# Kernel tuning notes

Measured on AMD Instinct MI355X. Metric: run time of the kernel, lower is better.

The kernel has to match this reference:

```python
import jax, jax.numpy as jnp
import numpy as np

B, N, DIM, H = 512, 98, 512, 16
HD = DIM // H
WS = (2, 7, 7)  # window size; N == 2*7*7


def _relative_position_index(ws):
    d, h, w = ws
    coords = np.stack(np.meshgrid(np.arange(d), np.arange(h), np.arange(w), indexing='ij'))
    cf = coords.reshape(3, -1)  # [3, N]
    rel = cf[:, :, None] - cf[:, None, :]  # [3, N, N]
    rel = rel.transpose(1, 2, 0).astype(np.int64)
    rel[:, :, 0] += d - 1
    rel[:, :, 1] += h - 1
    rel[:, :, 2] += w - 1
    rel[:, :, 0] *= (2 * h - 1) * (2 * w - 1)
    rel[:, :, 1] *= 2 * w - 1
    return rel.sum(-1)  # [N, N] in [0, (2d-1)(2h-1)(2w-1))


def setup_inputs() -> dict:
    key = jax.random.key(0)
    ks = jax.random.split(key, 6)
    table_size = (2 * WS[0] - 1) * (2 * WS[1] - 1) * (2 * WS[2] - 1)  # 507
    return {
        'x': jax.random.normal(ks[0], (B, N, DIM), jnp.float32),
        'qkv_w': jax.random.normal(ks[1], (DIM, 3 * DIM), jnp.float32) * 0.02,
        'qkv_b': jnp.zeros((3 * DIM,), jnp.float32),
        'proj_w': jax.random.normal(ks[2], (DIM, DIM), jnp.float32) * 0.02,
        'proj_b': jnp.zeros((DIM,), jnp.float32),
        'bias_table': jax.random.normal(ks[3], (table_size, H), jnp.float32) * 0.02,
        'rel_index': jnp.asarray(_relative_position_index(WS)),
    }


def reference(x, qkv_w, qkv_b, proj_w, proj_b, bias_table, rel_index):
    b, n, c = x.shape
    scale = HD ** -0.5
    qkv = (x @ qkv_w + qkv_b).reshape(b, n, 3, H, HD)
    qkv = jnp.transpose(qkv, (2, 0, 3, 1, 4))  # [3, B, H, N, HD]
    q, k, v = qkv[0] * scale, qkv[1], qkv[2]
    attn = jnp.einsum('bhnd,bhmd->bhnm', q, k)  # [B, H, N, N]
    # gather relative position bias: [N,N] indices into [table, H] -> [H, N, N]
    bias = jnp.transpose(bias_table[rel_index], (2, 0, 1))
    attn = jax.nn.softmax(attn + bias[None], axis=-1)
    out = jnp.einsum('bhnm,bhmd->bhnd', attn, v)  # [B, H, N, HD]
    out = jnp.transpose(out, (0, 2, 1, 3)).reshape(b, n, c)
    return out @ proj_w + proj_b
```

## Files before the change

### kernel.cpp

```cpp
#include <hip/hip_runtime.h>

typedef unsigned short u16;
typedef __bf16 bf16x8 __attribute__((ext_vector_type(8)));
typedef float f32x4 __attribute__((ext_vector_type(4)));

typedef __attribute__((address_space(1))) const void* as1_cvp;
typedef __attribute__((address_space(3))) void* as3_vp;

__device__ __forceinline__ float b2f(u16 u) {
  union { unsigned int i; float f; } x; x.i = ((unsigned int)u) << 16; return x.f;
}
__device__ __forceinline__ u16 f2b(float f) {
  union { float f; unsigned int i; } x; x.f = f;
  unsigned int u = x.i;
  u += 0x7fffu + ((u >> 16) & 1u);
  return (u16)(u >> 16);
}


__global__ void k_detect(const u16* __restrict__ x, int* __restrict__ flag) {
  int t = threadIdx.x;
  int sane = 0;
#pragma unroll
  for (int i = 0; i < 8; ++i) {
    u16 u = x[t * 8 + i];
    int e = (u >> 7) & 0xFF;
    sane += (u == 0 || (e >= 100 && e <= 150)) ? 1 : 0;
  }
#pragma unroll
  for (int off = 32; off >= 1; off >>= 1) sane += __shfl_xor(sane, off);
  if (t == 0) *flag = (sane < 480) ? 1 : 0;
}

__global__ void k_convert_pack(const void* __restrict__ xin, u16* __restrict__ xp,
                               const int* __restrict__ flagp) {
  const int f = *flagp;
  const int t = threadIdx.x, ln = t & 63;
  const int u = blockIdx.x * 4 + (t >> 6);
  const long r = (long)(u >> 4) * 16 + (ln & 15);
  const int kbase = (u & 15) * 32 + (ln >> 4) * 8;
  u16* dst = xp + ((long)u * 64 + ln) * 8;
  if (f) {
    const float* src = (const float*)xin + r * 512 + kbase;
    float4 v0 = *(const float4*)src;
    float4 v1 = *(const float4*)(src + 4);
    ushort4 s0, s1;
    s0.x = f2b(v0.x); s0.y = f2b(v0.y); s0.z = f2b(v0.z); s0.w = f2b(v0.w);
    s1.x = f2b(v1.x); s1.y = f2b(v1.y); s1.z = f2b(v1.z); s1.w = f2b(v1.w);
    *(ushort4*)dst = s0; *(ushort4*)(dst + 4) = s1;
  } else {
    const u16* src = (const u16*)xin + r * 512 + kbase;
    *(ushort4*)dst = *(const ushort4*)src;
    *(ushort4*)(dst + 4) = *(const ushort4*)(src + 4);
  }
}

__global__ void k_pack_w(const void* __restrict__ W, u16* __restrict__ WP,
                         const int* __restrict__ flagp, int N) {
  const int f = *flagp;
  const int t = threadIdx.x, ln = t & 63;
  const int u = blockIdx.x * 4 + (t >> 6);
  const int n = (u >> 4) * 16 + (ln & 15);
  const int k0 = (u & 15) * 32 + (ln >> 4) * 8;
  u16 v[8];
#pragma unroll
  for (int j = 0; j < 8; ++j) {
    long idx = (long)(k0 + j) * N + n;
    v[j] = f ? f2b(((const float*)W)[idx]) : ((const u16*)W)[idx];
  }
  u16* dst = WP + ((long)u * 64 + ln) * 8;
  ushort4 s0; s0.x = v[0]; s0.y = v[1]; s0.z = v[2]; s0.w = v[3];
  ushort4 s1; s1.x = v[4]; s1.y = v[5]; s1.z = v[6]; s1.w = v[7];
  *(ushort4*)dst = s0; *(ushort4*)(dst + 4) = s1;
}

__global__ void k_biasfrag(const int* __restrict__ rel, const void* __restrict__ table,
                           u16* __restrict__ biasFrag, const int* __restrict__ flagp) {
  int t = blockIdx.x * 256 + threadIdx.x;
  int f = *flagp;
  int ln = t & 63, r2 = t >> 6;
  int tj = r2 & 7, r3 = r2 >> 3;
  int ti = r3 % 7, h = r3 / 7;
  int col = ln & 15, qrow = ln >> 4;
  int j = tj * 16 + col;
  u16 v[4];
#pragma unroll
  for (int r = 0; r < 4; ++r) {
    int i = ti * 16 + qrow * 4 + r; if (i > 97) i = 97;
    float val;
    if (j < 98) {
      int rr = rel[i * 98 + j];
      val = f ? ((const float*)table)[rr * 16 + h] : b2f(((const u16*)table)[rr * 16 + h]);
    } else {
      val = -1e30f;
    }
    v[r] = f2b(val);
  }
  ushort4 out; out.x = v[0]; out.y = v[1]; out.z = v[2]; out.w = v[3];
  *(ushort4*)(biasFrag + (long)t * 4) = out;
}

#define LOADSET(SA, SB, KC)                                                    \
  _Pragma("unroll") for (int mi = 0; mi < 4; ++mi) {                           \
    SA[mi][0] = *(const bf16x8*)(aB + mi * 16384 + (KC) * 1024);               \
    SA[mi][1] = *(const bf16x8*)(aB + mi * 16384 + (KC) * 1024 + 1024);        \
  }                                                                            \
  _Pragma("unroll") for (int ni = 0; ni < 4; ++ni) {                           \
    SB[ni][0] = *(const bf16x8*)(bB + ni * 16384 + (KC) * 1024);               \
    SB[ni][1] = *(const bf16x8*)(bB + ni * 16384 + (KC) * 1024 + 1024);        \
  }

#define MFMASET(SA, SB)                                                        \
  __builtin_amdgcn_s_setprio(1);                                               \
  _Pragma("unroll") for (int kk = 0; kk < 2; ++kk)                             \
  _Pragma("unroll") for (int mi = 0; mi < 4; ++mi)                             \
  _Pragma("unroll") for (int ni = 0; ni < 4; ++ni)                             \
      acc[mi][ni] = __builtin_amdgcn_mfma_f32_16x16x32_bf16(                   \
          SA[mi][kk], SB[ni][kk], acc[mi][ni], 0, 0, 0);                       \
  __builtin_amdgcn_s_setprio(0);

__global__ __launch_bounds__(256, 2) void k_gemm_direct(
    const u16* __restrict__ PA, const u16* __restrict__ PB,
    const void* __restrict__ bias, void* __restrict__ C,
    const int* __restrict__ flagp, int N, int out_follows_flag, int NBY) {
  const int f = *flagp;
  const int t = threadIdx.x, w = t >> 6, ln = t & 63;
  const int nwg = gridDim.x, cpx = nwg >> 3;
  const int wg = (blockIdx.x & 7) * cpx + (blockIdx.x >> 3);
  const long bm = (long)(wg / NBY) * 128, bn = (long)(wg % NBY) * 128;
  const int wm = w >> 1, wn = w & 1;
  const int col = ln & 15, qrow = ln >> 4;
  const char* aB = (const char*)PA + ((bm >> 4) + wm * 4) * 16384L + ln * 16;
  const char* bB = (const char*)PB + ((bn >> 4) + wn * 4) * 16384L + ln * 16;
  float bv[4];
#pragma unroll
  for (int ni = 0; ni < 4; ++ni) {
    long c = bn + wn * 64 + ni * 16 + col;
    bv[ni] = f ? ((const float*)bias)[c] : b2f(((const u16*)bias)[c]);
  }
  f32x4 acc[4][4] = {};
  bf16x8 aX[4][2], bX[4][2], aY[4][2], bY[4][2];
  LOADSET(aX, bX, 0)
  LOADSET(aY, bY, 2)
#pragma unroll
  for (int kc = 0; kc < 16; kc += 4) {
    MFMASET(aX, bX)
    if (kc + 4 < 16) { LOADSET(aX, bX, kc + 4) }
    MFMASET(aY, bY)
    if (kc + 6 < 16) { LOADSET(aY, bY, kc + 6) }
  }
  const int of = out_follows_flag ? f : 0;
#pragma unroll
  for (int mi = 0; mi < 4; ++mi)
#pragma unroll
    for (int ni = 0; ni < 4; ++ni)
#pragma unroll
      for (int r = 0; r < 4; ++r) {
        long row = bm + wm * 64 + mi * 16 + qrow * 4 + r;
        long c = bn + wn * 64 + ni * 16 + col;
        float v = acc[mi][ni][r] + bv[ni];
        if (of) ((float*)C)[row * N + c] = v;
        else    ((u16*)C)[row * N + c] = f2b(v);
      }
}

__global__ __launch_bounds__(256) void k_attn(
    const u16* __restrict__ qkv, const u16* __restrict__ biasFrag,
    u16* __restrict__ attnp) {
  __shared__ __align__(16) u16 Qs[112 * 32];
  __shared__ __align__(16) u16 Ks[128 * 32];
  __shared__ __align__(16) u16 Vt[32 * 136];
  __shared__ __align__(16) u16 Ps[4][16 * 136];
  const int b = blockIdx.x, h = blockIdx.y;
  const int t = threadIdx.x, w = t >> 6, ln = t & 63;
  const u16* qbase = qkv + (long)b * 98 * 1536 + h * 32;
  {
    const int gr = ln >> 2, gc = (ln & 3) * 8;
    for (int n = w; n < 7; n += 4) {
      int g = n * 16 + gr; if (g > 97) g = 97;
      __builtin_amdgcn_global_load_lds((as1_cvp)(const void*)(qbase + (long)g * 1536 + gc),
                                       (as3_vp)(Qs + n * 512), 16, 0, 0);
    }
    for (int n = w; n < 8; n += 4) {
      int g = n * 16 + gr; if (g > 97) g = 97;
      __builtin_amdgcn_global_load_lds((as1_cvp)(const void*)(qbase + 512 + (long)g * 1536 + gc),
                                       (as3_vp)(Ks + n * 512), 16, 0, 0);
    }
  }
  for (int z = t; z < 32 * 19; z += 256) {
    int d = z / 19, q = z % 19;
    *(unsigned int*)&Vt[d * 136 + 98 + q * 2] = 0u;
  }
  for (int idx = t; idx < 784; idx += 256) {
    int i = idx >> 3, c4 = (idx & 7) * 4;
    ushort4 v4 = *(const ushort4*)(qbase + 1024 + (long)i * 1536 + c4);
    Vt[(c4 + 0) * 136 + i] = v4.x;
    Vt[(c4 + 1) * 136 + i] = v4.y;
    Vt[(c4 + 2) * 136 + i] = v4.z;
    Vt[(c4 + 3) * 136 + i] = v4.w;
  }
  __syncthreads();
  const int col = ln & 15, qrow = ln >> 4;
  const float scale = 0.17677669529663687f;
  u16* Psw = &Ps[w][0];
  f32x4 o[2][2] = {{{0.f,0.f,0.f,0.f},{0.f,0.f,0.f,0.f}},{{0.f,0.f,0.f,0.f},{0.f,0.f,0.f,0.f}}};
  for (int tt = 0; tt < 2; ++tt) {
    const int ti = w + tt * 4;
    if (ti >= 7) break;
    const u16* bp = biasFrag + ((long)((h * 7 + ti) * 8) * 64 + ln) * 4;
    ushort4 bfv[8];
#pragma unroll
    for (int tj = 0; tj < 8; ++tj) bfv[tj] = *(const ushort4*)(bp + tj * 256);
    bf16x8 aq = *(const bf16x8*)&Qs[(ti * 16 + col) * 32 + qrow * 8];
    f32x4 s[8];
#pragma unroll
    for (int tj = 0; tj < 8; ++tj) {
      bf16x8 bk = *(const bf16x8*)&Ks[(tj * 16 + col) * 32 + qrow * 8];
      f32x4 z = {0.f, 0.f, 0.f, 0.f};
      s[tj] = __builtin_amdgcn_mfma_f32_16x16x32_bf16(aq, bk, z, 0, 0, 0);
    }
#pragma unroll
    for (int r = 0; r < 4; ++r) {
      float vals[8]; float m = -1e30f;
#pragma unroll
      for (int tj = 0; tj < 8; ++tj) {
        u16 bb = (r == 0) ? bfv[tj].x : (r == 1) ? bfv[tj].y : (r == 2) ? bfv[tj].z : bfv[tj].w;
        float v = fmaf(s[tj][r], scale, b2f(bb));
        vals[tj] = v; m = fmaxf(m, v);
      }
#pragma unroll
      for (int off = 1; off < 16; off <<= 1) m = fmaxf(m, __shfl_xor(m, off));
      float sum = 0.f;
#pragma unroll
      for (int tj = 0; tj < 8; ++tj) { vals[tj] = __expf(vals[tj] - m); sum += vals[tj]; }
#pragma unroll
      for (int off = 1; off < 16; off <<= 1) sum += __shfl_xor(sum, off);
      float inv = 1.f / sum;
      const int rt = qrow * 4 + r;
#pragma unroll
      for (int tj = 0; tj < 8; ++tj)
        Psw[rt * 136 + tj * 16 + col] = f2b(vals[tj] * inv);
    }
#pragma unroll
    for (int ks = 0; ks < 4; ++ks) {
      bf16x8 ap  = *(const bf16x8*)&Psw[col * 136 + ks * 32 + qrow * 8];
      bf16x8 bv0 = *(const bf16x8*)&Vt[col * 136 + ks * 32 + qrow * 8];
      bf16x8 bv1 = *(const bf16x8*)&Vt[(16 + col) * 136 + ks * 32 + qrow * 8];
      o[tt][0] = __builtin_amdgcn_mfma_f32_16x16x32_bf16(ap, bv0, o[tt][0], 0, 0, 0);
      o[tt][1] = __builtin_amdgcn_mfma_f32_16x16x32_bf16(ap, bv1, o[tt][1], 0, 0, 0);
    }
  }
  __syncthreads();
  u16* Os = Qs;
#pragma unroll
  for (int tt = 0; tt < 2; ++tt) {
    const int ti = w + tt * 4;
    if (ti >= 7) continue;
#pragma unroll
    for (int r = 0; r < 4; ++r) {
      const int i = ti * 16 + qrow * 4 + r;
      if (i < 98) {
        Os[i * 32 + col]      = f2b(o[tt][0][r]);
        Os[i * 32 + 16 + col] = f2b(o[tt][1][r]);
      }
    }
  }
  __syncthreads();
  for (int idx = t; idx < 392; idx += 256) {
    int i = idx >> 2, o = idx & 3;
    long r = (long)b * 98 + i;
    u16* dst = attnp + ((r >> 4) * 16 + h) * 512 + ((r & 15) + (o << 4)) * 8;
    const u16* src = &Os[i * 32 + o * 8];
    *(ushort4*)dst = *(const ushort4*)src;
    *(ushort4*)(dst + 4) = *(const ushort4*)(src + 4);
  }
}

extern "C" void kernel_launch(void* const* d_in, const int* in_sizes, int n_in,
                              void* d_out, int out_size, void* d_ws, size_t ws_size,
                              hipStream_t stream) {
  (void)in_sizes; (void)n_in; (void)out_size; (void)ws_size;
  char* p = (char*)d_ws;
  u16* qkvbuf   = (u16*)p;  p += 50176L * 1536 * 2;
  u16* attnbuf  = (u16*)p;  u16* xp = attnbuf; p += 50176L * 512 * 2;
  u16* wqkvP    = (u16*)p;  p += 1536L * 512 * 2;
  u16* wprojP   = (u16*)p;  p += 512L * 512 * 2;
  u16* biasFrag = (u16*)p;  p += 57344L * 4 * 2;
  int* flagp    = (int*)p;

  k_detect<<<1, 64, 0, stream>>>((const u16*)d_in[0], flagp);
  k_convert_pack<<<12544, 256, 0, stream>>>(d_in[0], xp, flagp);
  k_pack_w<<<384, 256, 0, stream>>>(d_in[1], wqkvP, flagp, 1536);
  k_pack_w<<<128, 256, 0, stream>>>(d_in[3], wprojP, flagp, 512);
  k_biasfrag<<<224, 256, 0, stream>>>((const int*)d_in[6], d_in[5], biasFrag, flagp);
  k_gemm_direct<<<dim3(392 * 12), 256, 0, stream>>>(xp, wqkvP, d_in[2], qkvbuf,
                                                    flagp, 1536, 0, 12);
  k_attn<<<dim3(512, 16), 256, 0, stream>>>(qkvbuf, biasFrag, attnbuf);
  k_gemm_direct<<<dim3(392 * 4), 256, 0, stream>>>(attnbuf, wprojP, d_in[4], d_out,
                                                   flagp, 512, 1, 4);
}
```

Measured before the change: 437.3 us.

## Fuse QKV projection into attention kernel per (batch, head) block

Each attention block now computes its own Q, K and V slice directly from the bf16 input and packed QKV weights using MFMA, then writes the results straight into shared memory. This removes the separate QKV GEMM and the large qkv intermediate buffer round-trip through global memory. The input conversion becomes a plain row-major fp32-to-bf16 pass with no packing. Blocks are remapped so that the batches sharing an XCD reuse their input rows in cache. The cost is that every block re-reads the full 98x512 input rows for its batch, 16 times per batch across heads, and the fused kernel uses more registers per thread.

```diff
diff --git a/kernel.cpp b/kernel.cpp
--- a/kernel.cpp
+++ b/kernel.cpp
@@ -17,7 +17,6 @@
   return (u16)(u >> 16);
 }
 
-
 __global__ void k_detect(const u16* __restrict__ x, int* __restrict__ flag) {
   int t = threadIdx.x;
   int sane = 0;
@@ -32,27 +31,13 @@
   if (t == 0) *flag = (sane < 480) ? 1 : 0;
 }
 
-__global__ void k_convert_pack(const void* __restrict__ xin, u16* __restrict__ xp,
-                               const int* __restrict__ flagp) {
-  const int f = *flagp;
-  const int t = threadIdx.x, ln = t & 63;
-  const int u = blockIdx.x * 4 + (t >> 6);
-  const long r = (long)(u >> 4) * 16 + (ln & 15);
-  const int kbase = (u & 15) * 32 + (ln >> 4) * 8;
-  u16* dst = xp + ((long)u * 64 + ln) * 8;
-  if (f) {
-    const float* src = (const float*)xin + r * 512 + kbase;
-    float4 v0 = *(const float4*)src;
-    float4 v1 = *(const float4*)(src + 4);
-    ushort4 s0, s1;
-    s0.x = f2b(v0.x); s0.y = f2b(v0.y); s0.z = f2b(v0.z); s0.w = f2b(v0.w);
-    s1.x = f2b(v1.x); s1.y = f2b(v1.y); s1.z = f2b(v1.z); s1.w = f2b(v1.w);
-    *(ushort4*)dst = s0; *(ushort4*)(dst + 4) = s1;
-  } else {
-    const u16* src = (const u16*)xin + r * 512 + kbase;
-    *(ushort4*)dst = *(const ushort4*)src;
-    *(ushort4*)(dst + 4) = *(const ushort4*)(src + 4);
-  }
+__global__ void k_convert(const void* __restrict__ xin, u16* __restrict__ xb,
+                          const int* __restrict__ flagp) {
+  if (!*flagp) return;
+  long i = ((long)blockIdx.x * 256 + threadIdx.x) * 4;
+  float4 v = *(const float4*)((const float*)xin + i);
+  u16* o = xb + i;
+  o[0] = f2b(v.x); o[1] = f2b(v.y); o[2] = f2b(v.z); o[3] = f2b(v.w);
 }
 
 __global__ void k_pack_w(const void* __restrict__ W, u16* __restrict__ WP,
@@ -164,43 +149,98 @@
       }
 }
 
-__global__ __launch_bounds__(256) void k_attn(
-    const u16* __restrict__ qkv, const u16* __restrict__ biasFrag,
-    u16* __restrict__ attnp) {
+#define LOADQ(AS0, AS1, BS, KC) do {                                           \
+    AS0 = *(const bf16x8*)(a0p + (KC) * 64);                                   \
+    AS1 = *(const bf16x8*)(a1p + (KC) * 64);                                   \
+    _Pragma("unroll") for (int nt = 0; nt < 6; ++nt)                           \
+      BS[nt] = *(const bf16x8*)(bB[nt] + (KC) * 1024);                         \
+  } while (0)
+
+#define MFMAQ(AS0, AS1, BS)                                                    \
+  __builtin_amdgcn_s_setprio(1);                                               \
+  _Pragma("unroll") for (int nt = 0; nt < 6; ++nt)                             \
+    acc[0][nt] = __builtin_amdgcn_mfma_f32_16x16x32_bf16(AS0, BS[nt],          \
+                                                         acc[0][nt], 0, 0, 0); \
+  if (has1) {                                                                  \
+    _Pragma("unroll") for (int nt = 0; nt < 6; ++nt)                           \
+      acc[1][nt] = __builtin_amdgcn_mfma_f32_16x16x32_bf16(AS1, BS[nt],        \
+                                                          acc[1][nt], 0, 0, 0);\
+  }                                                                            \
+  __builtin_amdgcn_s_setprio(0);
+
+__global__ __launch_bounds__(256, 3) void k_fused(
+    const u16* __restrict__ x_raw, const u16* __restrict__ x_conv,
+    const u16* __restrict__ WP, const void* __restrict__ qkvb,
+    const u16* __restrict__ biasFrag, u16* __restrict__ attnp,
+    const int* __restrict__ flagp) {
   __shared__ __align__(16) u16 Qs[112 * 32];
   __shared__ __align__(16) u16 Ks[128 * 32];
   __shared__ __align__(16) u16 Vt[32 * 136];
   __shared__ __align__(16) u16 Ps[4][16 * 136];
-  const int b = blockIdx.x, h = blockIdx.y;
+  const int f = *flagp;
+  const u16* X = f ? x_conv : x_raw;
   const int t = threadIdx.x, w = t >> 6, ln = t & 63;
-  const u16* qbase = qkv + (long)b * 98 * 1536 + h * 32;
-  {
-    const int gr = ln >> 2, gc = (ln & 3) * 8;
-    for (int n = w; n < 7; n += 4) {
-      int g = n * 16 + gr; if (g > 97) g = 97;
-      __builtin_amdgcn_global_load_lds((as1_cvp)(const void*)(qbase + (long)g * 1536 + gc),
-                                       (as3_vp)(Qs + n * 512), 16, 0, 0);
-    }
-    for (int n = w; n < 8; n += 4) {
-      int g = n * 16 + gr; if (g > 97) g = 97;
-      __builtin_amdgcn_global_load_lds((as1_cvp)(const void*)(qbase + 512 + (long)g * 1536 + gc),
-                                       (as3_vp)(Ks + n * 512), 16, 0, 0);
-    }
-  }
+  const int raw = blockIdx.x;
+  const int xcd = raw & 7, slot = raw >> 3;
+  const int b = xcd + 8 * (slot >> 4), h = slot & 15;
+  const long r0 = (long)b * 98;
+  const int col = ln & 15, qrow = ln >> 4;
+  const int has1 = (w < 3);
+
+  *(unsigned int*)&Ks[112 * 32 + t * 2] = 0u;
   for (int z = t; z < 32 * 19; z += 256) {
     int d = z / 19, q = z % 19;
     *(unsigned int*)&Vt[d * 136 + 98 + q * 2] = 0u;
   }
-  for (int idx = t; idx < 784; idx += 256) {
-    int i = idx >> 3, c4 = (idx & 7) * 4;
-    ushort4 v4 = *(const ushort4*)(qbase + 1024 + (long)i * 1536 + c4);
-    Vt[(c4 + 0) * 136 + i] = v4.x;
-    Vt[(c4 + 1) * 136 + i] = v4.y;
-    Vt[(c4 + 2) * 136 + i] = v4.z;
-    Vt[(c4 + 3) * 136 + i] = v4.w;
+
+  long R0 = r0 + w * 16 + (ln & 15);        if (R0 > 50175) R0 = 50175;
+  long R1 = r0 + (w + 4) * 16 + (ln & 15);  if (R1 > 50175) R1 = 50175;
+  const char* a0p = (const char*)X + R0 * 1024 + (qrow << 4);
+  const char* a1p = (const char*)X + R1 * 1024 + (qrow << 4);
+  const char* wb = (const char*)WP + ln * 16;
+  const char* bB[6];
+  bB[0] = wb + (long)(2 * h) * 16384;       bB[1] = wb + (long)(2 * h + 1) * 16384;
+  bB[2] = wb + (long)(32 + 2 * h) * 16384;  bB[3] = wb + (long)(33 + 2 * h) * 16384;
+  bB[4] = wb + (long)(64 + 2 * h) * 16384;  bB[5] = wb + (long)(65 + 2 * h) * 16384;
+
+  f32x4 acc[2][6] = {};
+  bf16x8 aX0, aX1, bXv[6], aY0, aY1, bYv[6];
+  LOADQ(aX0, aX1, bXv, 0);
+  LOADQ(aY0, aY1, bYv, 1);
+#pragma unroll
+  for (int kc = 0; kc < 16; kc += 2) {
+    MFMAQ(aX0, aX1, bXv)
+    if (kc + 2 < 16) LOADQ(aX0, aX1, bXv, kc + 2);
+    MFMAQ(aY0, aY1, bYv)
+    if (kc + 3 < 16) LOADQ(aY0, aY1, bYv, kc + 3);
+  }
+  float qb[6];
+  {
+    const int nb0 = h * 32;
+    const int nbs[6] = {nb0, nb0 + 16, 512 + nb0, 528 + nb0, 1024 + nb0, 1040 + nb0};
+#pragma unroll
+    for (int nt = 0; nt < 6; ++nt) {
+      int n = nbs[nt] + col;
+      qb[nt] = f ? ((const float*)qkvb)[n] : b2f(((const u16*)qkvb)[n]);
+    }
+  }
+#pragma unroll
+  for (int tt = 0; tt < 2; ++tt) {
+    if (tt == 1 && !has1) break;
+    const int ti = w + tt * 4;
+#pragma unroll
+    for (int nt = 0; nt < 6; ++nt)
+#pragma unroll
+      for (int r = 0; r < 4; ++r) {
+        const int i = ti * 16 + qrow * 4 + r;
+        const u16 hv = f2b(acc[tt][nt][r] + qb[nt]);
+        if (nt < 2)      Qs[i * 32 + nt * 16 + col] = hv;
+        else if (nt < 4) Ks[i * 32 + (nt - 2) * 16 + col] = hv;
+        else if (i < 98) Vt[((nt - 4) * 16 + col) * 136 + i] = hv;
+      }
   }
   __syncthreads();
-  const int col = ln & 15, qrow = ln >> 4;
+
   const float scale = 0.17677669529663687f;
   u16* Psw = &Ps[w][0];
   f32x4 o[2][2] = {{{0.f,0.f,0.f,0.f},{0.f,0.f,0.f,0.f}},{{0.f,0.f,0.f,0.f},{0.f,0.f,0.f,0.f}}};
@@ -267,10 +307,10 @@
   }
   __syncthreads();
   for (int idx = t; idx < 392; idx += 256) {
-    int i = idx >> 2, o = idx & 3;
+    int i = idx >> 2, oo = idx & 3;
     long r = (long)b * 98 + i;
-    u16* dst = attnp + ((r >> 4) * 16 + h) * 512 + ((r & 15) + (o << 4)) * 8;
-    const u16* src = &Os[i * 32 + o * 8];
+    u16* dst = attnp + ((r >> 4) * 16 + h) * 512 + ((r & 15) + (oo << 4)) * 8;
+    const u16* src = &Os[i * 32 + oo * 8];
     *(ushort4*)dst = *(const ushort4*)src;
     *(ushort4*)(dst + 4) = *(const ushort4*)(src + 4);
   }
@@ -281,21 +321,20 @@
                               hipStream_t stream) {
   (void)in_sizes; (void)n_in; (void)out_size; (void)ws_size;
   char* p = (char*)d_ws;
-  u16* qkvbuf   = (u16*)p;  p += 50176L * 1536 * 2;
-  u16* attnbuf  = (u16*)p;  u16* xp = attnbuf; p += 50176L * 512 * 2;
+  u16* xb       = (u16*)p;  p += 50176L * 512 * 2;
+  u16* attnbuf  = (u16*)p;  p += 50176L * 512 * 2;
   u16* wqkvP    = (u16*)p;  p += 1536L * 512 * 2;
   u16* wprojP   = (u16*)p;  p += 512L * 512 * 2;
   u16* biasFrag = (u16*)p;  p += 57344L * 4 * 2;
   int* flagp    = (int*)p;
 
   k_detect<<<1, 64, 0, stream>>>((const u16*)d_in[0], flagp);
-  k_convert_pack<<<12544, 256, 0, stream>>>(d_in[0], xp, flagp);
+  k_convert<<<25088, 256, 0, stream>>>(d_in[0], xb, flagp);
   k_pack_w<<<384, 256, 0, stream>>>(d_in[1], wqkvP, flagp, 1536);
   k_pack_w<<<128, 256, 0, stream>>>(d_in[3], wprojP, flagp, 512);
   k_biasfrag<<<224, 256, 0, stream>>>((const int*)d_in[6], d_in[5], biasFrag, flagp);
-  k_gemm_direct<<<dim3(392 * 12), 256, 0, stream>>>(xp, wqkvP, d_in[2], qkvbuf,
-                                                    flagp, 1536, 0, 12);
-  k_attn<<<dim3(512, 16), 256, 0, stream>>>(qkvbuf, biasFrag, attnbuf);
+  k_fused<<<dim3(8192), 256, 0, stream>>>((const u16*)d_in[0], xb, wqkvP, d_in[2],
+                                          biasFrag, attnbuf, flagp);
   k_gemm_direct<<<dim3(392 * 4), 256, 0, stream>>>(attnbuf, wprojP, d_in[4], d_out,
                                                    flagp, 512, 1, 4);
 }
```

New measurement: 460.2 us. 5.2% more time.

## Widen GEMM block tile to 128x256 with each wave owning all rows

Applied to the files above, without the earlier changes.

Changes the direct-from-global GEMM so each workgroup computes a 128x256 output tile and each of the four waves covers all 128 rows by 64 columns, instead of a 2x2 wave layout over a 128x128 tile. The k-pipeline now double-buffers one k-chunk at a time rather than two, and the launch grids are halved. The aim is more MFMA work per A-fragment load and fewer workgroups. The cost is 128 accumulator floats per lane, which raises register pressure, and all four waves now load the same A fragments.

```diff
diff --git a/kernel.cpp b/kernel.cpp
--- a/kernel.cpp
+++ b/kernel.cpp
@@ -100,23 +100,18 @@
   *(ushort4*)(biasFrag + (long)t * 4) = out;
 }
 
-#define LOADSET(SA, SB, KC)                                                    \
-  _Pragma("unroll") for (int mi = 0; mi < 4; ++mi) {                           \
-    SA[mi][0] = *(const bf16x8*)(aB + mi * 16384 + (KC) * 1024);               \
-    SA[mi][1] = *(const bf16x8*)(aB + mi * 16384 + (KC) * 1024 + 1024);        \
-  }                                                                            \
-  _Pragma("unroll") for (int ni = 0; ni < 4; ++ni) {                           \
-    SB[ni][0] = *(const bf16x8*)(bB + ni * 16384 + (KC) * 1024);               \
-    SB[ni][1] = *(const bf16x8*)(bB + ni * 16384 + (KC) * 1024 + 1024);        \
-  }
-
-#define MFMASET(SA, SB)                                                        \
+#define LOADSET8(SA, SB, KC)                                                   \
+  _Pragma("unroll") for (int mi = 0; mi < 8; ++mi)                             \
+    SA[mi] = *(const bf16x8*)(aB + (mi * 16 + (KC)) * 1024);                   \
+  _Pragma("unroll") for (int ni = 0; ni < 4; ++ni)                             \
+    SB[ni] = *(const bf16x8*)(bB + (ni * 16 + (KC)) * 1024);
+
+#define MFMASET8(SA, SB)                                                       \
   __builtin_amdgcn_s_setprio(1);                                               \
-  _Pragma("unroll") for (int kk = 0; kk < 2; ++kk)                             \
-  _Pragma("unroll") for (int mi = 0; mi < 4; ++mi)                             \
+  _Pragma("unroll") for (int mi = 0; mi < 8; ++mi)                             \
   _Pragma("unroll") for (int ni = 0; ni < 4; ++ni)                             \
       acc[mi][ni] = __builtin_amdgcn_mfma_f32_16x16x32_bf16(                   \
-          SA[mi][kk], SB[ni][kk], acc[mi][ni], 0, 0, 0);                       \
+          SA[mi], SB[ni], acc[mi][ni], 0, 0, 0);                               \
   __builtin_amdgcn_s_setprio(0);
 
 __global__ __launch_bounds__(256, 2) void k_gemm_direct(
@@ -127,37 +122,36 @@
   const int t = threadIdx.x, w = t >> 6, ln = t & 63;
   const int nwg = gridDim.x, cpx = nwg >> 3;
   const int wg = (blockIdx.x & 7) * cpx + (blockIdx.x >> 3);
-  const long bm = (long)(wg / NBY) * 128, bn = (long)(wg % NBY) * 128;
-  const int wm = w >> 1, wn = w & 1;
+  const long bm = (long)(wg / NBY) * 128, bn = (long)(wg % NBY) * 256;
   const int col = ln & 15, qrow = ln >> 4;
-  const char* aB = (const char*)PA + ((bm >> 4) + wm * 4) * 16384L + ln * 16;
-  const char* bB = (const char*)PB + ((bn >> 4) + wn * 4) * 16384L + ln * 16;
+  const char* aB = (const char*)PA + (bm >> 4) * 16384L + ln * 16;
+  const char* bB = (const char*)PB + ((bn >> 4) + w * 4) * 16384L + ln * 16;
   float bv[4];
 #pragma unroll
   for (int ni = 0; ni < 4; ++ni) {
-    long c = bn + wn * 64 + ni * 16 + col;
+    long c = bn + w * 64 + ni * 16 + col;
     bv[ni] = f ? ((const float*)bias)[c] : b2f(((const u16*)bias)[c]);
   }
-  f32x4 acc[4][4] = {};
-  bf16x8 aX[4][2], bX[4][2], aY[4][2], bY[4][2];
-  LOADSET(aX, bX, 0)
-  LOADSET(aY, bY, 2)
-#pragma unroll
-  for (int kc = 0; kc < 16; kc += 4) {
-    MFMASET(aX, bX)
-    if (kc + 4 < 16) { LOADSET(aX, bX, kc + 4) }
-    MFMASET(aY, bY)
-    if (kc + 6 < 16) { LOADSET(aY, bY, kc + 6) }
+  f32x4 acc[8][4] = {};
+  bf16x8 aX[8], bX[4], aY[8], bY[4];
+  LOADSET8(aX, bX, 0)
+  LOADSET8(aY, bY, 1)
+#pragma unroll
+  for (int kc = 0; kc < 16; kc += 2) {
+    MFMASET8(aX, bX)
+    if (kc + 2 < 16) { LOADSET8(aX, bX, kc + 2) }
+    MFMASET8(aY, bY)
+    if (kc + 3 < 16) { LOADSET8(aY, bY, kc + 3) }
   }
   const int of = out_follows_flag ? f : 0;
 #pragma unroll
-  for (int mi = 0; mi < 4; ++mi)
+  for (int mi = 0; mi < 8; ++mi)
 #pragma unroll
     for (int ni = 0; ni < 4; ++ni)
 #pragma unroll
       for (int r = 0; r < 4; ++r) {
-        long row = bm + wm * 64 + mi * 16 + qrow * 4 + r;
-        long c = bn + wn * 64 + ni * 16 + col;
+        long row = bm + mi * 16 + qrow * 4 + r;
+        long c = bn + w * 64 + ni * 16 + col;
         float v = acc[mi][ni][r] + bv[ni];
         if (of) ((float*)C)[row * N + c] = v;
         else    ((u16*)C)[row * N + c] = f2b(v);
@@ -293,9 +287,9 @@
   k_pack_w<<<384, 256, 0, stream>>>(d_in[1], wqkvP, flagp, 1536);
   k_pack_w<<<128, 256, 0, stream>>>(d_in[3], wprojP, flagp, 512);
   k_biasfrag<<<224, 256, 0, stream>>>((const int*)d_in[6], d_in[5], biasFrag, flagp);
-  k_gemm_direct<<<dim3(392 * 12), 256, 0, stream>>>(xp, wqkvP, d_in[2], qkvbuf,
-                                                    flagp, 1536, 0, 12);
+  k_gemm_direct<<<dim3(392 * 6), 256, 0, stream>>>(xp, wqkvP, d_in[2], qkvbuf,
+                                                   flagp, 1536, 0, 6);
   k_attn<<<dim3(512, 16), 256, 0, stream>>>(qkvbuf, biasFrag, attnbuf);
-  k_gemm_direct<<<dim3(392 * 4), 256, 0, stream>>>(attnbuf, wprojP, d_in[4], d_out,
-                                                   flagp, 512, 1, 4);
-}
+  k_gemm_direct<<<dim3(392 * 2), 256, 0, stream>>>(attnbuf, wprojP, d_in[4], d_out,
+                                                   flagp, 512, 1, 2);
+}
```

Result: slower. 587.1 us (+34.2%).
